# Kernel tuning notes

Hardware: AMD Instinct MI355X
Metric: run time of the kernel (lower is better)

## Reference

```python
import jax, jax.numpy as jnp
import numpy as np

N_NODES = 100000
N_EDGES = 1600000
D_IN = 128
D_OUT = 128
NEG_SLOPE = 0.01  # F.leaky_relu default

def setup_inputs() -> dict:
    key = jax.random.key(0)
    k1, k2, k3, k4, k5, k6 = jax.random.split(key, 6)
    stdv = 1.0 / np.sqrt(D_OUT)
    return {
        "node_features": jax.random.normal(k1, (N_NODES, D_IN), dtype=jnp.float32),
        "edge_row": jax.random.randint(k2, (N_EDGES,), 0, N_NODES),  # dest node per edge
        "edge_col": jax.random.randint(k3, (N_EDGES,), 0, N_NODES),  # src node per edge
        "edge_val": jax.random.uniform(k4, (N_EDGES,), dtype=jnp.float32),
        "weight": jax.random.uniform(k5, (D_IN, D_OUT), dtype=jnp.float32, minval=-stdv, maxval=stdv),
        "bias": jax.random.uniform(k6, (D_OUT,), dtype=jnp.float32, minval=-stdv, maxval=stdv),
    }

def reference(node_features, edge_row, edge_col, edge_val, weight, bias):
    # x = node_features @ W  -> [N, D_OUT]
    h = node_features @ weight
    # spmm(adj, h): gather source features, scale by edge value, scatter-add to dest
    msg = edge_val[:, None] * h[edge_col]                       # [E, D_OUT]
    out = jax.ops.segment_sum(msg, edge_row, num_segments=node_features.shape[0])
    out = out + bias
    out = jnp.where(out >= 0, out, NEG_SLOPE * out)             # leaky_relu
    # dropout p=0 -> identity
    return out
```

## Files before the change

kernel.cpp:

```cpp
#include <hip/hip_runtime.h>

#define DMODEL 128
#define NEG_SLOPE 0.01f
#define NPB 64
#define NBK_MAX 1600
#define CPAD 16
#define SBLK 256
#define CAP 1536
#define OCAP 65536

typedef unsigned int uint;
typedef unsigned short ushort_t;
typedef __attribute__((ext_vector_type(8))) short short8v;
typedef __attribute__((ext_vector_type(4))) float float4v;

__device__ inline ushort_t f2bf(float f) {
    uint u = __float_as_uint(f);
    u += 0x7FFFu + ((u >> 16) & 1u);
    return (ushort_t)(u >> 16);
}

__global__ __launch_bounds__(256) void k_pre(const float* __restrict__ W,
                                             ushort_t* __restrict__ Wt,
                                             int* __restrict__ cur,
                                             int ztot) {
    const int b = blockIdx.x;
    if (b < 64) {
        const int t = b * 256 + threadIdx.x;
        const int k = t >> 7, c = t & 127;
        Wt[(size_t)c * DMODEL + k] = f2bf(W[(size_t)k * DMODEL + c]);
    } else {
        const int i = (b - 64) * 256 + threadIdx.x;
        if (i < ztot) cur[i] = 0;
    }
}

__global__ __launch_bounds__(256) void k_gemm(const float* __restrict__ X,
                                              const ushort_t* __restrict__ Wt,
                                              ushort_t* __restrict__ H, int N) {
    __shared__ ushort_t Xs[64 * 128];
    const int t = threadIdx.x;
    const int row0 = blockIdx.x * 64;

#pragma unroll
    for (int i = 0; i < 8; ++i) {
        const int f = t + i * 256;
        const int r = f >> 5;
        const int c4 = f & 31;
        float4 v = make_float4(0.f, 0.f, 0.f, 0.f);
        if (row0 + r < N) v = *(const float4*)(X + (size_t)(row0 + r) * DMODEL + c4 * 4);
        ushort4 u;
        u.x = f2bf(v.x); u.y = f2bf(v.y); u.z = f2bf(v.z); u.w = f2bf(v.w);
        const int chunk = (c4 >> 1) ^ (r & 7);
        *(ushort4*)(Xs + r * 128 + chunk * 8 + (c4 & 1) * 4) = u;
    }
    __syncthreads();

    const int wid = t >> 6, lane = t & 63;
    const int lr = lane & 15;
    const int kg = lane >> 4;
    const int wr = wid * 16 + lr;
    const ushort_t* wtb = Wt + (size_t)lr * DMODEL + kg * 8;

    float4v acc[8] = {};
#pragma unroll
    for (int s = 0; s < 4; ++s) {
        const int chunk = (s * 4 + kg) ^ (lr & 7);
        const short8v af = *(const short8v*)(Xs + wr * 128 + chunk * 8);
#pragma unroll
        for (int c = 0; c < 8; ++c) {
            const short8v bf = *(const short8v*)(wtb + (size_t)c * 16 * DMODEL + s * 32);
            acc[c] = __builtin_amdgcn_mfma_f32_16x16x32_bf16(af, bf, acc[c], 0, 0, 0);
        }
    }

#pragma unroll
    for (int c = 0; c < 8; ++c) {
#pragma unroll
        for (int r = 0; r < 4; ++r) {
            const int row = row0 + wid * 16 + kg * 4 + r;
            if (row < N) H[(size_t)row * DMODEL + c * 16 + lr] = f2bf(acc[c][r]);
        }
    }
}

__global__ __launch_bounds__(1024) void k_scat(const int* __restrict__ er,
                                               const int* __restrict__ ec,
                                               const float* __restrict__ ev,
                                               int* __restrict__ cur,
                                               int* __restrict__ ocnt,
                                               int4* __restrict__ ovf,
                                               int2* __restrict__ packed0,
                                               int E, int NBK, int chunk) {
    __shared__ int lh[NBK_MAX];
    __shared__ int lb[NBK_MAX];
    const int t = threadIdx.x;
    for (int k = t; k < NBK; k += 1024) lh[k] = 0;
    __syncthreads();
    const int s0 = blockIdx.x * chunk;
    const int s1 = min(E, s0 + chunk);
    for (int i = s0 + t * 4; i < s1; i += 4096) {
        if (i + 3 < s1) {
            int4 r = *(const int4*)(er + i);
            atomicAdd(&lh[r.x >> 6], 1);
            atomicAdd(&lh[r.y >> 6], 1);
            atomicAdd(&lh[r.z >> 6], 1);
            atomicAdd(&lh[r.w >> 6], 1);
        } else {
            for (int q = i; q < s1; ++q) atomicAdd(&lh[er[q] >> 6], 1);
        }
    }
    __syncthreads();
    for (int k = t; k < NBK; k += 1024) {
        int c = lh[k];
        lb[k] = c ? atomicAdd(&cur[k * CPAD], c) : 0;
        lh[k] = 0;
    }
    __syncthreads();
    for (int i = s0 + t * 4; i < s1; i += 4096) {
        if (i + 3 < s1) {
            int4 r = *(const int4*)(er + i);
            int4 c = *(const int4*)(ec + i);
            float4 v = *(const float4*)(ev + i);
            int bkt, rl, slot;
#define SCAT1(RR, CC, VV)                                                     \
            bkt = (RR) >> 6; rl = (RR) & 63;                                  \
            slot = lb[bkt] + atomicAdd(&lh[bkt], 1);                          \
            if (slot < CAP)                                                   \
                packed0[(size_t)bkt * CAP + slot] =                           \
                    make_int2((rl << 17) | (CC), __float_as_int(VV));         \
            else {                                                            \
                int o = atomicAdd(ocnt, 1);                                   \
                if (o < OCAP) ovf[o] = make_int4(bkt, rl, (CC), __float_as_int(VV)); \
            }
            SCAT1(r.x, c.x, v.x)
            SCAT1(r.y, c.y, v.y)
            SCAT1(r.z, c.z, v.z)
            SCAT1(r.w, c.w, v.w)
        } else {
            for (int q = i; q < s1; ++q) {
                int rr = er[q];
                int bkt = rr >> 6, rl = rr & 63;
                int slot = lb[bkt] + atomicAdd(&lh[bkt], 1);
                if (slot < CAP)
                    packed0[(size_t)bkt * CAP + slot] =
                        make_int2((rl << 17) | ec[q], __float_as_int(ev[q]));
                else {
                    int o = atomicAdd(ocnt, 1);
                    if (o < OCAP) ovf[o] = make_int4(bkt, rl, ec[q], __float_as_int(ev[q]));
                }
            }
        }
    }
}

__global__ __launch_bounds__(256) void k_bagg2(const uint* __restrict__ Hb,
                                               const int* __restrict__ cur,
                                               const int* __restrict__ ocnt,
                                               const int4* __restrict__ ovf,
                                               const int2* __restrict__ packed0,
                                               const float* __restrict__ bias,
                                               float* __restrict__ out, int N) {
    __shared__ int2 srt[CAP];
    __shared__ int lcnt[NPB];
    __shared__ int lpref[NPB];
    __shared__ int lcur[NPB];
    const int t = threadIdx.x;
    const int b = blockIdx.x;
    if (t < NPB) { lcnt[t] = 0; lcur[t] = 0; }
    __syncthreads();

    const int cnt = cur[b * CPAD];
    const int staged = min(cnt, CAP);
    const int2* slab = packed0 + (size_t)b * CAP;

    int2 myent[6];
#pragma unroll
    for (int k = 0; k < 6; ++k) {
        const int i = t + k * 256;
        myent[k] = make_int2(0, 0);
        if (i < staged) {
            myent[k] = slab[i];
            atomicAdd(&lcnt[((uint)myent[k].x) >> 17], 1);
        }
    }
    __syncthreads();

    if (t < NPB) {
        int p = 0;
        for (int k = 0; k < t; ++k) p += lcnt[k];
        lpref[t] = p;
    }
    __syncthreads();

#pragma unroll
    for (int k = 0; k < 6; ++k) {
        const int i = t + k * 256;
        if (i < staged) {
            const int rl = ((uint)myent[k].x) >> 17;
            const int pos = lpref[rl] + atomicAdd(&lcur[rl], 1);
            srt[pos] = make_int2(myent[k].x & 0x1FFFF, myent[k].y);
        }
    }
    __syncthreads();

    const int wid = t >> 6, lane = t & 63;
    const int h = lane >> 5, sl = lane & 31;
    const float4 bv = ((const float4*)bias)[sl];
    const int oc = min(*ocnt, OCAP);

    for (int r = wid * 16; r < wid * 16 + 16; ++r) {
        const int node = b * NPB + r;
        if (node >= N) continue;
        const int m = lcnt[r], p0 = lpref[r];
        float4 acc = make_float4(0.f, 0.f, 0.f, 0.f);
        int jj = h;
        for (; jj + 6 < m; jj += 8) {
            const int2 e0 = srt[p0 + jj];
            const int2 e1 = srt[p0 + jj + 2];
            const int2 e2 = srt[p0 + jj + 4];
            const int2 e3 = srt[p0 + jj + 6];
            const uint2 g0 = ((const uint2*)(Hb + (size_t)e0.x * 64))[sl];
            const uint2 g1 = ((const uint2*)(Hb + (size_t)e1.x * 64))[sl];
            const uint2 g2 = ((const uint2*)(Hb + (size_t)e2.x * 64))[sl];
            const uint2 g3 = ((const uint2*)(Hb + (size_t)e3.x * 64))[sl];
            const float v0 = __int_as_float(e0.y);
            const float v1 = __int_as_float(e1.y);
            const float v2 = __int_as_float(e2.y);
            const float v3 = __int_as_float(e3.y);
            acc.x = fmaf(v0, __uint_as_float(g0.x << 16), acc.x);
            acc.y = fmaf(v0, __uint_as_float(g0.x & 0xffff0000u), acc.y);
            acc.z = fmaf(v0, __uint_as_float(g0.y << 16), acc.z);
            acc.w = fmaf(v0, __uint_as_float(g0.y & 0xffff0000u), acc.w);
            acc.x = fmaf(v1, __uint_as_float(g1.x << 16), acc.x);
            acc.y = fmaf(v1, __uint_as_float(g1.x & 0xffff0000u), acc.y);
            acc.z = fmaf(v1, __uint_as_float(g1.y << 16), acc.z);
            acc.w = fmaf(v1, __uint_as_float(g1.y & 0xffff0000u), acc.w);
            acc.x = fmaf(v2, __uint_as_float(g2.x << 16), acc.x);
            acc.y = fmaf(v2, __uint_as_float(g2.x & 0xffff0000u), acc.y);
            acc.z = fmaf(v2, __uint_as_float(g2.y << 16), acc.z);
            acc.w = fmaf(v2, __uint_as_float(g2.y & 0xffff0000u), acc.w);
            acc.x = fmaf(v3, __uint_as_float(g3.x << 16), acc.x);
            acc.y = fmaf(v3, __uint_as_float(g3.x & 0xffff0000u), acc.y);
            acc.z = fmaf(v3, __uint_as_float(g3.y << 16), acc.z);
            acc.w = fmaf(v3, __uint_as_float(g3.y & 0xffff0000u), acc.w);
        }
        for (; jj < m; jj += 2) {
            const int2 e0 = srt[p0 + jj];
            const uint2 g0 = ((const uint2*)(Hb + (size_t)e0.x * 64))[sl];
            const float v0 = __int_as_float(e0.y);
            acc.x = fmaf(v0, __uint_as_float(g0.x << 16), acc.x);
            acc.y = fmaf(v0, __uint_as_float(g0.x & 0xffff0000u), acc.y);
            acc.z = fmaf(v0, __uint_as_float(g0.y << 16), acc.z);
            acc.w = fmaf(v0, __uint_as_float(g0.y & 0xffff0000u), acc.w);
        }
        for (int i = 0; i < oc; ++i) {
            const int4 o4 = ovf[i];
            if (o4.x == b && o4.y == r && h == 0) {
                const float v = __int_as_float(o4.w);
                const uint2 g = ((const uint2*)(Hb + (size_t)o4.z * 64))[sl];
                acc.x = fmaf(v, __uint_as_float(g.x << 16), acc.x);
                acc.y = fmaf(v, __uint_as_float(g.x & 0xffff0000u), acc.y);
                acc.z = fmaf(v, __uint_as_float(g.y << 16), acc.z);
                acc.w = fmaf(v, __uint_as_float(g.y & 0xffff0000u), acc.w);
            }
        }
        acc.x += __shfl_xor(acc.x, 32);
        acc.y += __shfl_xor(acc.y, 32);
        acc.z += __shfl_xor(acc.z, 32);
        acc.w += __shfl_xor(acc.w, 32);
        if (h == 0) {
            float4 o;
            o.x = acc.x + bv.x; o.y = acc.y + bv.y;
            o.z = acc.z + bv.z; o.w = acc.w + bv.w;
            o.x = o.x >= 0.f ? o.x : NEG_SLOPE * o.x;
            o.y = o.y >= 0.f ? o.y : NEG_SLOPE * o.y;
            o.z = o.z >= 0.f ? o.z : NEG_SLOPE * o.z;
            o.w = o.w >= 0.f ? o.w : NEG_SLOPE * o.w;
            ((float4*)(out + (size_t)node * DMODEL))[sl] = o;
        }
    }
}

extern "C" void kernel_launch(void* const* d_in, const int* in_sizes, int n_in,
                              void* d_out, int out_size, void* d_ws, size_t ws_size,
                              hipStream_t stream) {
    const float* X    = (const float*)d_in[0];
    const int*   er   = (const int*)d_in[1];
    const int*   ec   = (const int*)d_in[2];
    const float* ev   = (const float*)d_in[3];
    const float* W    = (const float*)d_in[4];
    const float* bias = (const float*)d_in[5];
    float* out = (float*)d_out;

    const int N = in_sizes[0] / DMODEL;
    const int E = in_sizes[1];
    const int NBK = (N + NPB - 1) / NPB;

    char* ws = (char*)d_ws;
    size_t off = 0;
    auto alloc = [&](size_t bytes) {
        void* p = ws + off;
        off += (bytes + 127) & ~(size_t)127;
        return p;
    };
    ushort_t* H   = (ushort_t*)alloc((size_t)N * DMODEL * sizeof(ushort_t));
    ushort_t* Wt  = (ushort_t*)alloc((size_t)DMODEL * DMODEL * sizeof(ushort_t));
    int* cur      = (int*)alloc(((size_t)NBK * CPAD + 1) * sizeof(int));
    int* ocnt     = cur + (size_t)NBK * CPAD;
    int4* ovf     = (int4*)alloc((size_t)OCAP * sizeof(int4));
    int2* packed0 = (int2*)alloc((size_t)NBK * CAP * sizeof(int2));
    (void)ws_size;

    const int ztot = NBK * CPAD + 1;

    hipLaunchKernelGGL(k_pre, dim3(64 + (ztot + 255) / 256), dim3(256), 0, stream,
                       W, Wt, cur, ztot);

    hipLaunchKernelGGL(k_gemm, dim3((N + 63) / 64), dim3(256), 0, stream, X, Wt, H, N);
    const int chunk = ((((E + SBLK - 1) / SBLK) + 3) & ~3);
    hipLaunchKernelGGL(k_scat, dim3(SBLK), dim3(1024), 0, stream,
                       er, ec, ev, cur, ocnt, ovf, packed0, E, NBK, chunk);

    hipLaunchKernelGGL(k_bagg2, dim3(NBK), dim3(256), 0, stream,
                       (const uint*)H, cur, ocnt, ovf, packed0, bias, out, N);
}
```

Before: 149.2 us.

## Split each aggregation bucket across two blocks and deepen gather unroll

```diff
diff --git a/kernel.cpp b/kernel.cpp
--- a/kernel.cpp
+++ b/kernel.cpp
@@ -73,7 +73,6 @@
             acc[c] = __builtin_amdgcn_mfma_f32_16x16x32_bf16(af, bf, acc[c], 0, 0, 0);
         }
     }
-
 #pragma unroll
     for (int c = 0; c < 8; ++c) {
 #pragma unroll
@@ -154,6 +153,15 @@
     }
 }
 
+#define EDGE_FMA(EE, GG)                                                      \
+    {                                                                         \
+        const float v_ = __int_as_float((EE).y);                              \
+        acc.x = fmaf(v_, __uint_as_float((GG).x << 16), acc.x);               \
+        acc.y = fmaf(v_, __uint_as_float((GG).x & 0xffff0000u), acc.y);       \
+        acc.z = fmaf(v_, __uint_as_float((GG).y << 16), acc.z);               \
+        acc.w = fmaf(v_, __uint_as_float((GG).y & 0xffff0000u), acc.w);       \
+    }
+
 __global__ __launch_bounds__(256) void k_bagg2(const uint* __restrict__ Hb,
                                                const int* __restrict__ cur,
                                                const int* __restrict__ ocnt,
@@ -162,12 +170,14 @@
                                                const float* __restrict__ bias,
                                                float* __restrict__ out, int N) {
     __shared__ int2 srt[CAP];
-    __shared__ int lcnt[NPB];
-    __shared__ int lpref[NPB];
-    __shared__ int lcur[NPB];
+    __shared__ int lcnt[32];
+    __shared__ int lpref[32];
+    __shared__ int lcur[32];
     const int t = threadIdx.x;
-    const int b = blockIdx.x;
-    if (t < NPB) { lcnt[t] = 0; lcur[t] = 0; }
+    const int b = blockIdx.x >> 1;
+    const int half = blockIdx.x & 1;
+    const int rbase = half * 32;
+    if (t < 32) { lcnt[t] = 0; lcur[t] = 0; }
     __syncthreads();
 
     const int cnt = cur[b * CPAD];
@@ -178,15 +188,18 @@
 #pragma unroll
     for (int k = 0; k < 6; ++k) {
         const int i = t + k * 256;
-        myent[k] = make_int2(0, 0);
-        if (i < staged) {
-            myent[k] = slab[i];
-            atomicAdd(&lcnt[((uint)myent[k].x) >> 17], 1);
-        }
-    }
-    __syncthreads();
-
-    if (t < NPB) {
+        myent[k] = (i < staged) ? slab[i] : make_int2(-1, 0);
+    }
+#pragma unroll
+    for (int k = 0; k < 6; ++k) {
+        if (myent[k].x >= 0) {
+            const int rl = ((uint)myent[k].x) >> 17;
+            if (rl >= rbase && rl < rbase + 32) atomicAdd(&lcnt[rl - rbase], 1);
+        }
+    }
+    __syncthreads();
+
+    if (t < 32) {
         int p = 0;
         for (int k = 0; k < t; ++k) p += lcnt[k];
         lpref[t] = p;
@@ -195,11 +208,13 @@
 
 #pragma unroll
     for (int k = 0; k < 6; ++k) {
-        const int i = t + k * 256;
-        if (i < staged) {
+        if (myent[k].x >= 0) {
             const int rl = ((uint)myent[k].x) >> 17;
-            const int pos = lpref[rl] + atomicAdd(&lcur[rl], 1);
-            srt[pos] = make_int2(myent[k].x & 0x1FFFF, myent[k].y);
+            if (rl >= rbase && rl < rbase + 32) {
+                const int lr = rl - rbase;
+                const int pos = lpref[lr] + atomicAdd(&lcur[lr], 1);
+                srt[pos] = make_int2(myent[k].x & 0x1FFFF, myent[k].y);
+            }
         }
     }
     __syncthreads();
@@ -209,12 +224,32 @@
     const float4 bv = ((const float4*)bias)[sl];
     const int oc = min(*ocnt, OCAP);
 
-    for (int r = wid * 16; r < wid * 16 + 16; ++r) {
-        const int node = b * NPB + r;
+    for (int r = wid * 8; r < wid * 8 + 8; ++r) {
+        const int node = b * NPB + rbase + r;
         if (node >= N) continue;
         const int m = lcnt[r], p0 = lpref[r];
         float4 acc = make_float4(0.f, 0.f, 0.f, 0.f);
         int jj = h;
+        for (; jj + 14 < m; jj += 16) {
+            const int2 e0 = srt[p0 + jj];
+            const int2 e1 = srt[p0 + jj + 2];
+            const int2 e2 = srt[p0 + jj + 4];
+            const int2 e3 = srt[p0 + jj + 6];
+            const int2 e4 = srt[p0 + jj + 8];
+            const int2 e5 = srt[p0 + jj + 10];
+            const int2 e6 = srt[p0 + jj + 12];
+            const int2 e7 = srt[p0 + jj + 14];
+            const uint2 g0 = ((const uint2*)(Hb + (size_t)e0.x * 64))[sl];
+            const uint2 g1 = ((const uint2*)(Hb + (size_t)e1.x * 64))[sl];
+            const uint2 g2 = ((const uint2*)(Hb + (size_t)e2.x * 64))[sl];
+            const uint2 g3 = ((const uint2*)(Hb + (size_t)e3.x * 64))[sl];
+            const uint2 g4 = ((const uint2*)(Hb + (size_t)e4.x * 64))[sl];
+            const uint2 g5 = ((const uint2*)(Hb + (size_t)e5.x * 64))[sl];
+            const uint2 g6 = ((const uint2*)(Hb + (size_t)e6.x * 64))[sl];
+            const uint2 g7 = ((const uint2*)(Hb + (size_t)e7.x * 64))[sl];
+            EDGE_FMA(e0, g0) EDGE_FMA(e1, g1) EDGE_FMA(e2, g2) EDGE_FMA(e3, g3)
+            EDGE_FMA(e4, g4) EDGE_FMA(e5, g5) EDGE_FMA(e6, g6) EDGE_FMA(e7, g7)
+        }
         for (; jj + 6 < m; jj += 8) {
             const int2 e0 = srt[p0 + jj];
             const int2 e1 = srt[p0 + jj + 2];
@@ -224,39 +259,16 @@
             const uint2 g1 = ((const uint2*)(Hb + (size_t)e1.x * 64))[sl];
             const uint2 g2 = ((const uint2*)(Hb + (size_t)e2.x * 64))[sl];
             const uint2 g3 = ((const uint2*)(Hb + (size_t)e3.x * 64))[sl];
-            const float v0 = __int_as_float(e0.y);
-            const float v1 = __int_as_float(e1.y);
-            const float v2 = __int_as_float(e2.y);
-            const float v3 = __int_as_float(e3.y);
-            acc.x = fmaf(v0, __uint_as_float(g0.x << 16), acc.x);
-            acc.y = fmaf(v0, __uint_as_float(g0.x & 0xffff0000u), acc.y);
-            acc.z = fmaf(v0, __uint_as_float(g0.y << 16), acc.z);
-            acc.w = fmaf(v0, __uint_as_float(g0.y & 0xffff0000u), acc.w);
-            acc.x = fmaf(v1, __uint_as_float(g1.x << 16), acc.x);
-            acc.y = fmaf(v1, __uint_as_float(g1.x & 0xffff0000u), acc.y);
-            acc.z = fmaf(v1, __uint_as_float(g1.y << 16), acc.z);
-            acc.w = fmaf(v1, __uint_as_float(g1.y & 0xffff0000u), acc.w);
-            acc.x = fmaf(v2, __uint_as_float(g2.x << 16), acc.x);
-            acc.y = fmaf(v2, __uint_as_float(g2.x & 0xffff0000u), acc.y);
-            acc.z = fmaf(v2, __uint_as_float(g2.y << 16), acc.z);
-            acc.w = fmaf(v2, __uint_as_float(g2.y & 0xffff0000u), acc.w);
-            acc.x = fmaf(v3, __uint_as_float(g3.x << 16), acc.x);
-            acc.y = fmaf(v3, __uint_as_float(g3.x & 0xffff0000u), acc.y);
-            acc.z = fmaf(v3, __uint_as_float(g3.y << 16), acc.z);
-            acc.w = fmaf(v3, __uint_as_float(g3.y & 0xffff0000u), acc.w);
+            EDGE_FMA(e0, g0) EDGE_FMA(e1, g1) EDGE_FMA(e2, g2) EDGE_FMA(e3, g3)
         }
         for (; jj < m; jj += 2) {
             const int2 e0 = srt[p0 + jj];
             const uint2 g0 = ((const uint2*)(Hb + (size_t)e0.x * 64))[sl];
-            const float v0 = __int_as_float(e0.y);
-            acc.x = fmaf(v0, __uint_as_float(g0.x << 16), acc.x);
-            acc.y = fmaf(v0, __uint_as_float(g0.x & 0xffff0000u), acc.y);
-            acc.z = fmaf(v0, __uint_as_float(g0.y << 16), acc.z);
-            acc.w = fmaf(v0, __uint_as_float(g0.y & 0xffff0000u), acc.w);
+            EDGE_FMA(e0, g0)
         }
         for (int i = 0; i < oc; ++i) {
             const int4 o4 = ovf[i];
-            if (o4.x == b && o4.y == r && h == 0) {
+            if (o4.x == b && o4.y == rbase + r && h == 0) {
                 const float v = __int_as_float(o4.w);
                 const uint2 g = ((const uint2*)(Hb + (size_t)o4.z * 64))[sl];
                 acc.x = fmaf(v, __uint_as_float(g.x << 16), acc.x);
@@ -322,6 +334,6 @@
     hipLaunchKernelGGL(k_scat, dim3(SBLK), dim3(1024), 0, stream,
                        er, ec, ev, cur, ocnt, ovf, packed0, E, NBK, chunk);
 
-    hipLaunchKernelGGL(k_bagg2, dim3(NBK), dim3(256), 0, stream,
+    hipLaunchKernelGGL(k_bagg2, dim3(2 * NBK), dim3(256), 0, stream,
                        (const uint*)H, cur, ocnt, ovf, packed0, bias, out, N);
 }
```

Result: no change. 149.7 us (+0.3%).
